# Performance work log

Hardware: AMD Instinct MI355X
Metric: run time of the kernel (lower is better)

## Reference

```python
import jax, jax.numpy as jnp
import numpy as np

N = 50000
E = 800000
F0, F1, F2 = 256, 128, 64
EPS = 1e-5


def setup_inputs() -> dict:
    key = jax.random.key(0)
    ks = jax.random.split(key, 20)
    x = jax.random.normal(ks[0], (N, F0), dtype=jnp.float32)
    src = jax.random.randint(ks[1], (E,), 0, N)
    dst = jax.random.randint(ks[2], (E,), 0, N)
    edge_index = jnp.stack([src, dst]).astype(jnp.int64)

    def lin(k, fi, fo):
        s = 1.0 / np.sqrt(fi)
        k1, k2 = jax.random.split(k)
        W = jax.random.uniform(k1, (fi, fo), minval=-s, maxval=s, dtype=jnp.float32)
        b = jax.random.uniform(k2, (fo,), minval=-s, maxval=s, dtype=jnp.float32)
        return W, b

    We1, be1 = lin(ks[3], F0, F1)
    We2, be2 = lin(ks[4], F1, F2)
    Wd1, bd1 = lin(ks[5], F2, F1)
    Wd2, bd2 = lin(ks[6], F1, F0)
    return {
        'x': x, 'edge_index': edge_index,
        'We1': We1, 'be1': be1, 'g1': jnp.ones((F1,)), 'bb1': jnp.zeros((F1,)),
        'We2': We2, 'be2': be2, 'g2': jnp.ones((F2,)), 'bb2': jnp.zeros((F2,)),
        'Wd1': Wd1, 'bd1': bd1, 'g3': jnp.ones((F1,)), 'bb3': jnp.zeros((F1,)),
        'Wd2': Wd2, 'bd2': bd2, 'g4': jnp.ones((F0,)), 'bb4': jnp.zeros((F0,)),
    }


def _gcn(x, W, b, src, dst, dinv_src_dst, dinv_self):
    # PyG GCNConv: linear first, then sym-normalized propagation with self-loops
    h = x @ W + b                               # [N, Fout]
    msg = h[src] * dinv_src_dst[:, None]        # [E, Fout]
    out = jax.ops.segment_sum(msg, dst, num_segments=N)
    return out + h * dinv_self[:, None]         # self-loop term


def _bn(x, g, b):
    # BatchNorm1d training-mode: biased batch stats over node dim
    m = jnp.mean(x, axis=0)
    v = jnp.mean(jnp.square(x - m), axis=0)
    return g * (x - m) * jax.lax.rsqrt(v + EPS) + b


def reference(x, edge_index, We1, be1, g1, bb1, We2, be2, g2, bb2,
              Wd1, bd1, g3, bb3, Wd2, bd2, g4, bb4):
    src, dst = edge_index[0], edge_index[1]
    deg = jnp.zeros((N,), x.dtype).at[dst].add(1.0) + 1.0  # in-degree + self-loop
    dinv = jax.lax.rsqrt(deg)
    dsd = dinv[src] * dinv[dst]
    dself = dinv * dinv

    relu = jax.nn.relu
    # Encoder block 0 (outer i==0): relu(GCN), relu(BN)
    h = relu(_gcn(x, We1, be1, src, dst, dsd, dself))
    h = relu(_bn(h, g1, bb1))
    enc1 = h
    # Encoder block 1 (outer i==1 == len(inner)-1): relu(GCN), BN (no relu)
    h = relu(_gcn(h, We2, be2, src, dst, dsd, dself))
    h = _bn(h, g2, bb2)
    enc2 = h
    # Decoder block 0: relu(GCN), relu(BN)
    h = relu(_gcn(h, Wd1, bd1, src, dst, dsd, dself))
    h = relu(_bn(h, g3, bb3))
    # Decoder block 1 (i==1): relu(GCN), BN (no relu)
    h = relu(_gcn(h, Wd2, bd2, src, dst, dsd, dself))
    h = _bn(h, g4, bb4)
    # AE returns (reconstruction, encoded_embeddings)
    return h, enc1, enc2
```

## Files before the change

### kernel.cpp

```cpp
#include <hip/hip_runtime.h>

#define N_NODES 50000
#define F0 256
#define F1 128
#define F2 64
#define BN_EPS 1e-5f

typedef float f32x4 __attribute__((ext_vector_type(4)));
typedef __bf16 bf16x8 __attribute__((ext_vector_type(8)));
typedef unsigned short ushort8v __attribute__((ext_vector_type(8)));

__device__ __forceinline__ float bflo(unsigned v) { return __uint_as_float(v << 16); }
__device__ __forceinline__ float bfhi(unsigned v) { return __uint_as_float(v & 0xFFFF0000u); }
__device__ __forceinline__ unsigned short f2bf(float f) {
  unsigned u = __float_as_uint(f);
  u += 0x7FFFu + ((u >> 16) & 1u);
  return (unsigned short)(u >> 16);
}
__device__ __forceinline__ void split2(float a, unsigned short& hi, unsigned short& lo) {
  hi = f2bf(a);
  float hf = __uint_as_float((unsigned)hi << 16);
  lo = f2bf(a - hf);
}
__device__ __forceinline__ int rdl(int v, int l) { return __builtin_amdgcn_readlane(v, l); }
__device__ __forceinline__ float rdlf(float v, int l) {
  return __uint_as_float((unsigned)__builtin_amdgcn_readlane(__float_as_int(v), l));
}

__global__ void count_dst(const int* __restrict__ dst, int* __restrict__ counts, int E) {
  int e = blockIdx.x * blockDim.x + threadIdx.x;
  if (e < E) atomicAdd(&counts[dst[e]], 1);
}

__global__ __launch_bounds__(256) void scan_blocks(const int* __restrict__ counts,
                                                   int* __restrict__ offs,
                                                   int* __restrict__ bsum,
                                                   float* __restrict__ dinv) {
  __shared__ int s_w[4];
  const int tid = threadIdx.x, lane = tid & 63, wid = tid >> 6;
  const int base = blockIdx.x * 1024 + tid * 4;
  int v0 = 0, v1 = 0, v2 = 0, v3 = 0;
  if (base + 3 < N_NODES) {
    int4 v = *(const int4*)(counts + base);
    v0 = v.x; v1 = v.y; v2 = v.z; v3 = v.w;
  } else if (base < N_NODES) {
    v0 = counts[base];
    if (base + 1 < N_NODES) v1 = counts[base + 1];
    if (base + 2 < N_NODES) v2 = counts[base + 2];
  }
  if (base < N_NODES) {
    dinv[base] = rsqrtf((float)v0 + 1.0f);
    if (base + 1 < N_NODES) dinv[base + 1] = rsqrtf((float)v1 + 1.0f);
    if (base + 2 < N_NODES) dinv[base + 2] = rsqrtf((float)v2 + 1.0f);
    if (base + 3 < N_NODES) dinv[base + 3] = rsqrtf((float)v3 + 1.0f);
  }
  int t = v0 + v1 + v2 + v3;
  int incl = t;
#pragma unroll
  for (int d = 1; d < 64; d <<= 1) {
    int x = __shfl_up(incl, d);
    if (lane >= d) incl += x;
  }
  if (lane == 63) s_w[wid] = incl;
  __syncthreads();
  int woff = 0;
#pragma unroll
  for (int j = 0; j < 4; j++)
    if (j < wid) woff += s_w[j];
  int p = woff + incl - t;
  if (base < N_NODES) offs[base] = p;
  p += v0;
  if (base + 1 < N_NODES) offs[base + 1] = p;
  p += v1;
  if (base + 2 < N_NODES) offs[base + 2] = p;
  p += v2;
  if (base + 3 < N_NODES) offs[base + 3] = p;
  if (tid == 255) bsum[blockIdx.x] = woff + incl;
}

__global__ void scan_tops(int* __restrict__ bsum, int* __restrict__ offs, int nblk) {
  int lane = threadIdx.x;
  int v = (lane < nblk) ? bsum[lane] : 0;
  int incl = v;
#pragma unroll
  for (int d = 1; d < 64; d <<= 1) {
    int x = __shfl_up(incl, d);
    if (lane >= d) incl += x;
  }
  if (lane < nblk) bsum[lane] = incl - v;
  if (lane == 63) offs[N_NODES] = incl;
}

__global__ __launch_bounds__(256) void scan_add(int* __restrict__ offs,
                                                const int* __restrict__ bsum,
                                                const float* __restrict__ dinv,
                                                float* __restrict__ rowsum) {
  const int add = bsum[blockIdx.x];
  const int base = blockIdx.x * 1024 + threadIdx.x * 4;
  if (base + 3 < N_NODES) {
    int4 v = *(const int4*)(offs + base);
    v.x += add; v.y += add; v.z += add; v.w += add;
    *(int4*)(offs + base) = v;
    float4 d = *(const float4*)(dinv + base);
    float4 r;
    r.x = d.x * d.x; r.y = d.y * d.y; r.z = d.z * d.z; r.w = d.w * d.w;
    *(float4*)(rowsum + base) = r;
  } else if (base < N_NODES) {
    for (int k = 0; k < 4 && base + k < N_NODES; k++) {
      offs[base + k] += add;
      float d = dinv[base + k];
      rowsum[base + k] = d * d;
    }
  }
}

__global__ void fill_csr(const int* __restrict__ src, const int* __restrict__ dst,
                         const int* __restrict__ offs, int* __restrict__ cursor,
                         const float* __restrict__ dinv,
                         int* __restrict__ csr_src, float* __restrict__ csr_w,
                         float* __restrict__ rowsum, int E) {
  int e = blockIdx.x * blockDim.x + threadIdx.x;
  if (e < E) {
    int s = src[e], d = dst[e];
    int p = offs[d] + atomicAdd(&cursor[d], 1);
    float w = dinv[s] * dinv[d];
    csr_src[p] = s;
    csr_w[p] = w;
    atomicAdd(&rowsum[d], w);
  }
}

__device__ __forceinline__ void wt_one(const float* W, unsigned short* Wh, unsigned short* Wl,
                                       int K, int N, int idx) {
  int k = idx / N, n = idx - k * N;
  unsigned short h, l;
  split2(W[idx], h, l);
  Wh[(size_t)n * K + k] = h;
  Wl[(size_t)n * K + k] = l;
}

__global__ void convert_weights(const float* __restrict__ We1, const float* __restrict__ We2,
                                const float* __restrict__ Wd1, const float* __restrict__ Wd2,
                                unsigned short* W1h, unsigned short* W1l,
                                unsigned short* W2h, unsigned short* W2l,
                                unsigned short* W3h, unsigned short* W3l,
                                unsigned short* W4h, unsigned short* W4l) {
  int idx = blockIdx.x * blockDim.x + threadIdx.x;
  if (idx < 32768) {
    wt_one(We1, W1h, W1l, 256, 128, idx);
  } else if (idx < 40960) {
    wt_one(We2, W2h, W2l, 128, 64, idx - 32768);
  } else if (idx < 49152) {
    wt_one(Wd1, W3h, W3l, 64, 128, idx - 40960);
  } else if (idx < 81920) {
    wt_one(Wd2, W4h, W4l, 128, 256, idx - 49152);
  }
}

template <int BN, bool STATS, bool AF32>
__global__ __launch_bounds__(256) void mfma_gemm_split(
    const unsigned short* __restrict__ Ahi, const unsigned short* __restrict__ Alo,
    const float* __restrict__ Af,
    const unsigned short* __restrict__ Whi, const unsigned short* __restrict__ Wlo,
    const float* __restrict__ bias, const float* __restrict__ rowsum,
    unsigned short* __restrict__ Cb, float* __restrict__ Cf,
    float* __restrict__ stat, int M, int K, int N) {
  constexpr int BM = 128;
  constexpr int MT = (BN == 128) ? 4 : 2;
  constexpr int NT = 4;
  __shared__ __align__(16) unsigned short AsH[4][BM][8];
  __shared__ __align__(16) unsigned short AsL[4][BM][8];
  __shared__ __align__(16) unsigned short BsH[4][BN][8];
  __shared__ __align__(16) unsigned short BsL[4][BN][8];
  const int tid = threadIdx.x;
  const int lane = tid & 63, wid = tid >> 6;
  const int quad = lane >> 4, ln = lane & 15;
  const int m0 = blockIdx.x * BM;
  const int n0 = blockIdx.y * BN;
  const int wm = (BN == 128) ? (wid & 1) * 64 : wid * 32;
  const int wn = (BN == 128) ? (wid >> 1) * 64 : 0;
  f32x4 acc[MT][NT] = {};

  const int arow = tid >> 2, aseg = tid & 3;
  for (int k0 = 0; k0 < K; k0 += 32) {
#pragma unroll
    for (int i = 0; i < 2; i++) {
      int row = arow + i * 64;
      int gm = m0 + row;
      if (AF32) {
        float4 u0 = make_float4(0.f, 0.f, 0.f, 0.f), u1 = u0;
        if (gm < M) {
          u0 = *(const float4*)(Af + (size_t)gm * K + k0 + aseg * 8);
          u1 = *(const float4*)(Af + (size_t)gm * K + k0 + aseg * 8 + 4);
        }
        ushort4 h0, l0, h1, l1;
        split2(u0.x, h0.x, l0.x); split2(u0.y, h0.y, l0.y);
        split2(u0.z, h0.z, l0.z); split2(u0.w, h0.w, l0.w);
        split2(u1.x, h1.x, l1.x); split2(u1.y, h1.y, l1.y);
        split2(u1.z, h1.z, l1.z); split2(u1.w, h1.w, l1.w);
        *(ushort4*)(&AsH[aseg][row][0]) = h0;
        *(ushort4*)(&AsH[aseg][row][4]) = h1;
        *(ushort4*)(&AsL[aseg][row][0]) = l0;
        *(ushort4*)(&AsL[aseg][row][4]) = l1;
      } else {
        ushort8v vh = {0, 0, 0, 0, 0, 0, 0, 0};
        ushort8v vl = {0, 0, 0, 0, 0, 0, 0, 0};
        if (gm < M) {
          vh = *(const ushort8v*)(Ahi + (size_t)gm * K + k0 + aseg * 8);
          vl = *(const ushort8v*)(Alo + (size_t)gm * K + k0 + aseg * 8);
        }
        *(ushort8v*)(&AsH[aseg][row][0]) = vh;
        *(ushort8v*)(&AsL[aseg][row][0]) = vl;
      }
    }
#pragma unroll
    for (int i = 0; i < BN / 64; i++) {
      int n = arow + i * 64;
      *(ushort8v*)(&BsH[aseg][n][0]) =
          *(const ushort8v*)(Whi + (size_t)(n0 + n) * K + k0 + aseg * 8);
      *(ushort8v*)(&BsL[aseg][n][0]) =
          *(const ushort8v*)(Wlo + (size_t)(n0 + n) * K + k0 + aseg * 8);
    }
    __syncthreads();
    bf16x8 ah[MT], al[MT], bh[NT], bl[NT];
#pragma unroll
    for (int mt = 0; mt < MT; mt++) {
      ah[mt] = *(const bf16x8*)(&AsH[quad][wm + mt * 16 + ln][0]);
      al[mt] = *(const bf16x8*)(&AsL[quad][wm + mt * 16 + ln][0]);
    }
#pragma unroll
    for (int nt = 0; nt < NT; nt++) {
      bh[nt] = *(const bf16x8*)(&BsH[quad][wn + nt * 16 + ln][0]);
      bl[nt] = *(const bf16x8*)(&BsL[quad][wn + nt * 16 + ln][0]);
    }
#pragma unroll
    for (int mt = 0; mt < MT; mt++)
#pragma unroll
      for (int nt = 0; nt < NT; nt++) {
        acc[mt][nt] = __builtin_amdgcn_mfma_f32_16x16x32_bf16(ah[mt], bl[nt], acc[mt][nt], 0, 0, 0);
        acc[mt][nt] = __builtin_amdgcn_mfma_f32_16x16x32_bf16(al[mt], bh[nt], acc[mt][nt], 0, 0, 0);
        acc[mt][nt] = __builtin_amdgcn_mfma_f32_16x16x32_bf16(ah[mt], bh[nt], acc[mt][nt], 0, 0, 0);
      }
    __syncthreads();
  }

  if (!STATS) {
#pragma unroll
    for (int nt = 0; nt < NT; nt++) {
      int gn = n0 + wn + nt * 16 + ln;
      float bv = bias[gn];
#pragma unroll
      for (int mt = 0; mt < MT; mt++) {
#pragma unroll
        for (int r = 0; r < 4; r++) {
          int gm = m0 + wm + mt * 16 + quad * 4 + r;
          if (gm < M) Cb[(size_t)gm * N + gn] = f2bf(acc[mt][nt][r] + bv);
        }
      }
    }
  } else {
    float rs[MT][4];
#pragma unroll
    for (int mt = 0; mt < MT; mt++)
#pragma unroll
      for (int r = 0; r < 4; r++) {
        int gm = m0 + wm + mt * 16 + quad * 4 + r;
        rs[mt][r] = (gm < M) ? rowsum[gm] : 0.f;
      }
#pragma unroll
    for (int nt = 0; nt < NT; nt++) {
      int gn = n0 + wn + nt * 16 + ln;
      float bv = bias[gn];
      float ls = 0.f, lq = 0.f;
#pragma unroll
      for (int mt = 0; mt < MT; mt++) {
#pragma unroll
        for (int r = 0; r < 4; r++) {
          int gm = m0 + wm + mt * 16 + quad * 4 + r;
          if (gm < M) {
            float v = fmaxf(fmaf(bv, rs[mt][r], acc[mt][nt][r]), 0.f);
            Cf[(size_t)gm * N + gn] = v;
            ls += v;
            lq = fmaf(v, v, lq);
          }
        }
      }
      ls += __shfl_xor(ls, 16); ls += __shfl_xor(ls, 32);
      lq += __shfl_xor(lq, 16); lq += __shfl_xor(lq, 32);
      if (quad == 0) {
        atomicAdd(&stat[gn], ls);
        atomicAdd(&stat[256 + gn], lq);
      }
    }
  }
}

template <bool RELU_STATS, bool OUT_SPLIT>
__global__ __launch_bounds__(256) void agg128_rl(
    const unsigned short* __restrict__ hb, const int* __restrict__ offs,
    const int* __restrict__ csr_src, const float* __restrict__ csr_w,
    const float* __restrict__ dinv, float* __restrict__ outf,
    unsigned short* __restrict__ outhi, unsigned short* __restrict__ outlo,
    float* __restrict__ stat) {
  const int tid = threadIdx.x;
  const int lane = tid & 63;
  const int widx = tid >> 6;
  const int nwaves = gridDim.x * 4;
  float ls0 = 0.f, ls1 = 0.f, lq0 = 0.f, lq1 = 0.f;

  for (int node = blockIdx.x * 4 + widx; node < N_NODES; node += nwaves) {
    const int e0 = __builtin_amdgcn_readfirstlane(offs[node]);
    const int e1 = __builtin_amdgcn_readfirstlane(offs[node + 1]);
    float a0 = 0.f, a1 = 0.f;
    for (int e = e0; e < e1; e += 64) {
      const int cnt = min(64, e1 - e);
      int idx = 0;
      float wt = 0.f;
      if (lane < cnt) {
        idx = csr_src[e + lane];
        wt = csr_w[e + lane];
      }
      const int nb = (cnt + 7) & ~7;
      for (int j = 0; j < nb; j += 8) {
#pragma unroll
        for (int u = 0; u < 8; u++) {
          int s = rdl(idx, j + u);
          float w = rdlf(wt, j + u);
          unsigned v = *(const unsigned*)(hb + (size_t)s * 128 + lane * 2);
          a0 = fmaf(bflo(v), w, a0);
          a1 = fmaf(bfhi(v), w, a1);
        }
      }
    }
    float di = dinv[node];
    float ds = di * di;
    unsigned vs = *(const unsigned*)(hb + (size_t)node * 128 + lane * 2);
    a0 = fmaf(bflo(vs), ds, a0);
    a1 = fmaf(bfhi(vs), ds, a1);
    if (RELU_STATS) {
      a0 = fmaxf(a0, 0.f);
      a1 = fmaxf(a1, 0.f);
      ls0 += a0; ls1 += a1;
      lq0 = fmaf(a0, a0, lq0);
      lq1 = fmaf(a1, a1, lq1);
    }
    if (OUT_SPLIT) {
      unsigned short h0, l0, h1, l1;
      split2(a0, h0, l0);
      split2(a1, h1, l1);
      *(unsigned*)(outhi + (size_t)node * 128 + lane * 2) = (unsigned)h0 | ((unsigned)h1 << 16);
      *(unsigned*)(outlo + (size_t)node * 128 + lane * 2) = (unsigned)l0 | ((unsigned)l1 << 16);
    } else {
      *(float2*)(outf + (size_t)node * 128 + lane * 2) = make_float2(a0, a1);
    }
  }

  if (RELU_STATS) {
    __shared__ float red[4][128];
    red[widx][lane * 2 + 0] = ls0;
    red[widx][lane * 2 + 1] = ls1;
    __syncthreads();
    if (tid < 128) {
      atomicAdd(&stat[tid], red[0][tid] + red[1][tid] + red[2][tid] + red[3][tid]);
    }
    __syncthreads();
    red[widx][lane * 2 + 0] = lq0;
    red[widx][lane * 2 + 1] = lq1;
    __syncthreads();
    if (tid < 128) {
      atomicAdd(&stat[256 + tid], red[0][tid] + red[1][tid] + red[2][tid] + red[3][tid]);
    }
  }
}

template <bool RELU_STATS, bool OUT_SPLIT>
__global__ __launch_bounds__(256) void agg64_rl(
    const unsigned short* __restrict__ hb, const int* __restrict__ offs,
    const int* __restrict__ csr_src, const float* __restrict__ csr_w,
    const float* __restrict__ dinv, float* __restrict__ outf,
    unsigned short* __restrict__ outhi, unsigned short* __restrict__ outlo,
    float* __restrict__ stat) {
  const int tid = threadIdx.x;
  const int lane = tid & 63;
  const int widx = tid >> 6;
  const int half = lane >> 5;
  const int hl = lane & 31;
  const int nwaves = gridDim.x * 4;
  float ls0 = 0.f, ls1 = 0.f, lq0 = 0.f, lq1 = 0.f;

  for (int node = blockIdx.x * 4 + widx; node < N_NODES; node += nwaves) {
    const int e0 = __builtin_amdgcn_readfirstlane(offs[node]);
    const int e1 = __builtin_amdgcn_readfirstlane(offs[node + 1]);
    float a0 = 0.f, a1 = 0.f;
    for (int e = e0; e < e1; e += 64) {
      const int cnt = min(64, e1 - e);
      int idx = 0;
      float wt = 0.f;
      if (lane < cnt) {
        idx = csr_src[e + lane];
        wt = csr_w[e + lane];
      }
      const int nb = (cnt + 15) & ~15;
      for (int j = 0; j < nb; j += 16) {
#pragma unroll
        for (int u = 0; u < 8; u++) {
          int sa = rdl(idx, j + 2 * u);
          int sb = rdl(idx, j + 2 * u + 1);
          float wa = rdlf(wt, j + 2 * u);
          float wb = rdlf(wt, j + 2 * u + 1);
          const unsigned short* pa = hb + (size_t)sa * 64;
          const unsigned short* pb = hb + (size_t)sb * 64;
          const unsigned short* p = half ? pb : pa;
          float w = half ? wb : wa;
          unsigned v = *(const unsigned*)(p + hl * 2);
          a0 = fmaf(bflo(v), w, a0);
          a1 = fmaf(bfhi(v), w, a1);
        }
      }
    }
    a0 += __shfl_xor(a0, 32);
    a1 += __shfl_xor(a1, 32);
    float di = dinv[node];
    float ds = di * di;
    unsigned vs = *(const unsigned*)(hb + (size_t)node * 64 + hl * 2);
    a0 = fmaf(bflo(vs), ds, a0);
    a1 = fmaf(bfhi(vs), ds, a1);
    if (RELU_STATS) {
      a0 = fmaxf(a0, 0.f);
      a1 = fmaxf(a1, 0.f);
      if (half == 0) {
        ls0 += a0; ls1 += a1;
        lq0 = fmaf(a0, a0, lq0);
        lq1 = fmaf(a1, a1, lq1);
      }
    }
    if (half == 0) {
      if (OUT_SPLIT) {
        unsigned short h0, l0, h1, l1;
        split2(a0, h0, l0);
        split2(a1, h1, l1);
        *(unsigned*)(outhi + (size_t)node * 64 + hl * 2) = (unsigned)h0 | ((unsigned)h1 << 16);
        *(unsigned*)(outlo + (size_t)node * 64 + hl * 2) = (unsigned)l0 | ((unsigned)l1 << 16);
      } else {
        *(float2*)(outf + (size_t)node * 64 + hl * 2) = make_float2(a0, a1);
      }
    }
  }

  if (RELU_STATS) {
    __shared__ float red[4][64];
    if (half == 0) {
      red[widx][hl * 2 + 0] = ls0;
      red[widx][hl * 2 + 1] = ls1;
    }
    __syncthreads();
    if (tid < 64) {
      atomicAdd(&stat[tid], red[0][tid] + red[1][tid] + red[2][tid] + red[3][tid]);
    }
    __syncthreads();
    if (half == 0) {
      red[widx][hl * 2 + 0] = lq0;
      red[widx][hl * 2 + 1] = lq1;
    }
    __syncthreads();
    if (tid < 64) {
      atomicAdd(&stat[256 + tid], red[0][tid] + red[1][tid] + red[2][tid] + red[3][tid]);
    }
  }
}

template <int F, bool RELU, bool WF32, bool WB16, bool WSPLIT>
__global__ __launch_bounds__(256) void bn_apply_f(const float* __restrict__ a,
                                                  const float* __restrict__ stat,
                                                  const float* __restrict__ g,
                                                  const float* __restrict__ bb,
                                                  float* __restrict__ outf,
                                                  unsigned short* __restrict__ outb,
                                                  unsigned short* __restrict__ outhi,
                                                  unsigned short* __restrict__ outlo) {
  __shared__ float s_scale[F], s_shift[F];
  const int tid = threadIdx.x;
  if (tid < F) {
    const float invN = 1.0f / (float)N_NODES;
    float mean = stat[tid] * invN;
    float var = fmaxf(stat[256 + tid] * invN - mean * mean, 0.f);
    float inv = rsqrtf(var + BN_EPS);
    float sc = g[tid] * inv;
    s_scale[tid] = sc;
    s_shift[tid] = bb[tid] - mean * sc;
  }
  __syncthreads();
  constexpr int C4 = F / 4;
  const int total = N_NODES * C4;
  for (int idx = blockIdx.x * blockDim.x + tid; idx < total; idx += gridDim.x * blockDim.x) {
    int c4 = idx % C4;
    float4 v = ((const float4*)a)[idx];
    float4 s = *(float4*)&s_scale[c4 * 4];
    float4 sh = *(float4*)&s_shift[c4 * 4];
    float4 o;
    o.x = fmaf(v.x, s.x, sh.x);
    o.y = fmaf(v.y, s.y, sh.y);
    o.z = fmaf(v.z, s.z, sh.z);
    o.w = fmaf(v.w, s.w, sh.w);
    if (RELU) {
      o.x = fmaxf(o.x, 0.f);
      o.y = fmaxf(o.y, 0.f);
      o.z = fmaxf(o.z, 0.f);
      o.w = fmaxf(o.w, 0.f);
    }
    if (WF32) ((float4*)outf)[idx] = o;
    if (WB16) {
      ushort4 b;
      b.x = f2bf(o.x); b.y = f2bf(o.y); b.z = f2bf(o.z); b.w = f2bf(o.w);
      ((ushort4*)outb)[idx] = b;
    }
    if (WSPLIT) {
      ushort4 h, l;
      split2(o.x, h.x, l.x);
      split2(o.y, h.y, l.y);
      split2(o.z, h.z, l.z);
      split2(o.w, h.w, l.w);
      ((ushort4*)outhi)[idx] = h;
      ((ushort4*)outlo)[idx] = l;
    }
  }
}

extern "C" void kernel_launch(void* const* d_in, const int* in_sizes, int n_in,
                              void* d_out, int out_size, void* d_ws, size_t ws_size,
                              hipStream_t stream) {
  const float* x = (const float*)d_in[0];
  const int* ei = (const int*)d_in[1];
  const int E = in_sizes[1] / 2;
  const int* src = ei;
  const int* dst = ei + E;
  const float* We1 = (const float*)d_in[2];  const float* be1 = (const float*)d_in[3];
  const float* g1  = (const float*)d_in[4];  const float* bb1 = (const float*)d_in[5];
  const float* We2 = (const float*)d_in[6];  const float* be2 = (const float*)d_in[7];
  const float* g2  = (const float*)d_in[8];  const float* bb2 = (const float*)d_in[9];
  const float* Wd1 = (const float*)d_in[10]; const float* bd1 = (const float*)d_in[11];
  const float* g3  = (const float*)d_in[12]; const float* bb3 = (const float*)d_in[13];
  const float* Wd2 = (const float*)d_in[14]; const float* bd2 = (const float*)d_in[15];
  const float* g4  = (const float*)d_in[16]; const float* bb4 = (const float*)d_in[17];

  float* out = (float*)d_out;
  char* ws = (char*)d_ws;
  unsigned short* A0b  = (unsigned short*)(ws + 0);
  unsigned short* A1b  = (unsigned short*)(ws + 12800000);
  unsigned short* C2b  = (unsigned short*)(ws + 32000000);
  unsigned short* G3hi = (unsigned short*)(ws + 0);
  unsigned short* G3lo = (unsigned short*)(ws + 6400000);
  unsigned short* D3b  = (unsigned short*)(ws + 12800000);
  unsigned short* G4hi = (unsigned short*)(ws + 0);
  unsigned short* G4lo = (unsigned short*)(ws + 25600000);
  unsigned short* Wb   = (unsigned short*)(ws + 48000000);
  unsigned short* W1h = Wb;            unsigned short* W1l = W1h + 32768;
  unsigned short* W2h = W1l + 32768;   unsigned short* W2l = W2h + 8192;
  unsigned short* W3h = W2l + 8192;    unsigned short* W3l = W3h + 8192;
  unsigned short* W4h = W3l + 8192;    unsigned short* W4l = W4h + 32768;
  float* B0f  = (float*)(ws + 51200000);
  int*   csrS   = (int*)(ws + 102400000);
  float* csrW   = (float*)(ws + 105600000);
  float* stat4  = (float*)(ws + 108800000);
  int*   bsum   = (int*)(ws + 108808192);
  int*   counts = (int*)(ws + 108810000);
  int*   cursor = (int*)(ws + 109010000);
  int*   offs   = (int*)(ws + 109210000);
  float* dinv   = (float*)(ws + 109410064);
  if (ws_size < 109604160) return;
  float* rowsum = (float*)counts;

  float* enc1 = out + (size_t)N_NODES * F0;
  float* enc2 = enc1 + (size_t)N_NODES * F1;

  const int EB = (E + 255) / 256;
  const int AGG_GRID = 2048;
  const int MB = (N_NODES + 127) / 128;
  const int SCAN_B = (N_NODES + 1023) / 1024;

  convert_weights<<<320, 256, 0, stream>>>(We1, We2, Wd1, Wd2, W1h, W1l, W2h, W2l,
                                           W3h, W3l, W4h, W4l);
  hipMemsetAsync(counts, 0, 400000, stream);
  hipMemsetAsync(stat4, 0, 4 * 512 * sizeof(float), stream);
  count_dst<<<EB, 256, 0, stream>>>(dst, counts, E);
  scan_blocks<<<SCAN_B, 256, 0, stream>>>(counts, offs, bsum, dinv);
  scan_tops<<<1, 64, 0, stream>>>(bsum, offs, SCAN_B);
  scan_add<<<SCAN_B, 256, 0, stream>>>(offs, bsum, dinv, rowsum);
  fill_csr<<<EB, 256, 0, stream>>>(src, dst, offs, cursor, dinv, csrS, csrW, rowsum, E);

  mfma_gemm_split<128, false, true><<<dim3(MB, 1), 256, 0, stream>>>(
      nullptr, nullptr, x, W1h, W1l, be1, nullptr, A0b, nullptr, nullptr, N_NODES, F0, F1);
  agg128_rl<true, false><<<AGG_GRID, 256, 0, stream>>>(
      A0b, offs, csrS, csrW, dinv, B0f, nullptr, nullptr, stat4);
  bn_apply_f<F1, true, true, false, false><<<2048, 256, 0, stream>>>(
      B0f, stat4, g1, bb1, enc1, nullptr, nullptr, nullptr);

  mfma_gemm_split<64, false, true><<<dim3(MB, 1), 256, 0, stream>>>(
      nullptr, nullptr, enc1, W2h, W2l, be2, nullptr, A1b, nullptr, nullptr, N_NODES, F1, F2);
  agg64_rl<true, false><<<AGG_GRID, 256, 0, stream>>>(
      A1b, offs, csrS, csrW, dinv, B0f, nullptr, nullptr, stat4 + 512);
  bn_apply_f<F2, false, true, true, false><<<2048, 256, 0, stream>>>(
      B0f, stat4 + 512, g2, bb2, enc2, C2b, nullptr, nullptr);

  agg64_rl<false, true><<<AGG_GRID, 256, 0, stream>>>(
      C2b, offs, csrS, csrW, dinv, nullptr, G3hi, G3lo, nullptr);
  mfma_gemm_split<128, true, false><<<dim3(MB, 1), 256, 0, stream>>>(
      G3hi, G3lo, nullptr, W3h, W3l, bd1, rowsum, nullptr, B0f, stat4 + 1024, N_NODES, F2, F1);
  bn_apply_f<F1, true, false, true, false><<<2048, 256, 0, stream>>>(
      B0f, stat4 + 1024, g3, bb3, nullptr, D3b, nullptr, nullptr);

  agg128_rl<false, true><<<AGG_GRID, 256, 0, stream>>>(
      D3b, offs, csrS, csrW, dinv, nullptr, G4hi, G4lo, nullptr);
  mfma_gemm_split<128, true, false><<<dim3(MB, 2), 256, 0, stream>>>(
      G4hi, G4lo, nullptr, W4h, W4l, bd2, rowsum, nullptr, B0f, stat4 + 1536, N_NODES, F1, F0);
  bn_apply_f<F0, false, true, false, false><<<2048, 256, 0, stream>>>(
      B0f, stat4 + 1536, g4, bb4, out, nullptr, nullptr, nullptr);
}
```

Baseline: 639.4 us.

## Pack CSR entries as 64-bit pairs and reuse count-phase atomic slots

The count pass now records each edge's atomic slot, so fill_csr no longer needs a second atomic cursor pass or the cursor memset. The CSR source index and weight are packed into one 64-bit entry written with nontemporal stores, so each aggregation kernel does one load per edge instead of two. The atomic rowsum accumulation is replaced by a separate per-node kernel that sums weights from the CSR. This adds a serial per-thread loop in compute_rowsum and an extra launch, and eslot aliases the B0f buffer.

```diff
diff --git a/kernel.cpp b/kernel.cpp
--- a/kernel.cpp
+++ b/kernel.cpp
@@ -27,9 +27,10 @@
   return __uint_as_float((unsigned)__builtin_amdgcn_readlane(__float_as_int(v), l));
 }
 
-__global__ void count_dst(const int* __restrict__ dst, int* __restrict__ counts, int E) {
+__global__ void count_dst(const int* __restrict__ dst, int* __restrict__ counts,
+                          int* __restrict__ eslot, int E) {
   int e = blockIdx.x * blockDim.x + threadIdx.x;
-  if (e < E) atomicAdd(&counts[dst[e]], 1);
+  if (e < E) eslot[e] = atomicAdd(&counts[dst[e]], 1);
 }
 
 __global__ __launch_bounds__(256) void scan_blocks(const int* __restrict__ counts,
@@ -92,41 +93,43 @@
 }
 
 __global__ __launch_bounds__(256) void scan_add(int* __restrict__ offs,
-                                                const int* __restrict__ bsum,
-                                                const float* __restrict__ dinv,
-                                                float* __restrict__ rowsum) {
+                                                const int* __restrict__ bsum) {
   const int add = bsum[blockIdx.x];
   const int base = blockIdx.x * 1024 + threadIdx.x * 4;
   if (base + 3 < N_NODES) {
     int4 v = *(const int4*)(offs + base);
     v.x += add; v.y += add; v.z += add; v.w += add;
     *(int4*)(offs + base) = v;
-    float4 d = *(const float4*)(dinv + base);
-    float4 r;
-    r.x = d.x * d.x; r.y = d.y * d.y; r.z = d.z * d.z; r.w = d.w * d.w;
-    *(float4*)(rowsum + base) = r;
   } else if (base < N_NODES) {
-    for (int k = 0; k < 4 && base + k < N_NODES; k++) {
-      offs[base + k] += add;
-      float d = dinv[base + k];
-      rowsum[base + k] = d * d;
-    }
+    offs[base] += add;
+    if (base + 1 < N_NODES) offs[base + 1] += add;
+    if (base + 2 < N_NODES) offs[base + 2] += add;
   }
 }
 
 __global__ void fill_csr(const int* __restrict__ src, const int* __restrict__ dst,
-                         const int* __restrict__ offs, int* __restrict__ cursor,
+                         const int* __restrict__ offs, const int* __restrict__ eslot,
                          const float* __restrict__ dinv,
-                         int* __restrict__ csr_src, float* __restrict__ csr_w,
-                         float* __restrict__ rowsum, int E) {
+                         unsigned long long* __restrict__ csrP, int E) {
   int e = blockIdx.x * blockDim.x + threadIdx.x;
   if (e < E) {
     int s = src[e], d = dst[e];
-    int p = offs[d] + atomicAdd(&cursor[d], 1);
-    float w = dinv[s] * dinv[d];
-    csr_src[p] = s;
-    csr_w[p] = w;
-    atomicAdd(&rowsum[d], w);
+    int p = offs[d] + eslot[e];
+    unsigned long long ent =
+        (unsigned)s | ((unsigned long long)__float_as_uint(dinv[s] * dinv[d]) << 32);
+    __builtin_nontemporal_store(ent, &csrP[p]);
+  }
+}
+
+__global__ void compute_rowsum(const int* __restrict__ offs,
+                               const unsigned long long* __restrict__ csrP,
+                               const float* __restrict__ dinv, float* __restrict__ rowsum) {
+  int i = blockIdx.x * blockDim.x + threadIdx.x;
+  if (i < N_NODES) {
+    float s = dinv[i] * dinv[i];
+    int e1 = offs[i + 1];
+    for (int e = offs[i]; e < e1; e++) s += __uint_as_float((unsigned)(csrP[e] >> 32));
+    rowsum[i] = s;
   }
 }
 
@@ -298,10 +301,9 @@
 template <bool RELU_STATS, bool OUT_SPLIT>
 __global__ __launch_bounds__(256) void agg128_rl(
     const unsigned short* __restrict__ hb, const int* __restrict__ offs,
-    const int* __restrict__ csr_src, const float* __restrict__ csr_w,
-    const float* __restrict__ dinv, float* __restrict__ outf,
-    unsigned short* __restrict__ outhi, unsigned short* __restrict__ outlo,
-    float* __restrict__ stat) {
+    const unsigned long long* __restrict__ csrP, const float* __restrict__ dinv,
+    float* __restrict__ outf, unsigned short* __restrict__ outhi,
+    unsigned short* __restrict__ outlo, float* __restrict__ stat) {
   const int tid = threadIdx.x;
   const int lane = tid & 63;
   const int widx = tid >> 6;
@@ -317,8 +319,9 @@
       int idx = 0;
       float wt = 0.f;
       if (lane < cnt) {
-        idx = csr_src[e + lane];
-        wt = csr_w[e + lane];
+        unsigned long long c = csrP[e + lane];
+        idx = (int)(unsigned)c;
+        wt = __uint_as_float((unsigned)(c >> 32));
       }
       const int nb = (cnt + 7) & ~7;
       for (int j = 0; j < nb; j += 8) {
@@ -376,10 +379,9 @@
 template <bool RELU_STATS, bool OUT_SPLIT>
 __global__ __launch_bounds__(256) void agg64_rl(
     const unsigned short* __restrict__ hb, const int* __restrict__ offs,
-    const int* __restrict__ csr_src, const float* __restrict__ csr_w,
-    const float* __restrict__ dinv, float* __restrict__ outf,
-    unsigned short* __restrict__ outhi, unsigned short* __restrict__ outlo,
-    float* __restrict__ stat) {
+    const unsigned long long* __restrict__ csrP, const float* __restrict__ dinv,
+    float* __restrict__ outf, unsigned short* __restrict__ outhi,
+    unsigned short* __restrict__ outlo, float* __restrict__ stat) {
   const int tid = threadIdx.x;
   const int lane = tid & 63;
   const int widx = tid >> 6;
@@ -397,8 +399,9 @@
       int idx = 0;
       float wt = 0.f;
       if (lane < cnt) {
-        idx = csr_src[e + lane];
-        wt = csr_w[e + lane];
+        unsigned long long c = csrP[e + lane];
+        idx = (int)(unsigned)c;
+        wt = __uint_as_float((unsigned)(c >> 32));
       }
       const int nb = (cnt + 15) & ~15;
       for (int j = 0; j < nb; j += 16) {
@@ -559,12 +562,11 @@
   unsigned short* W3h = W2l + 8192;    unsigned short* W3l = W3h + 8192;
   unsigned short* W4h = W3l + 8192;    unsigned short* W4l = W4h + 32768;
   float* B0f  = (float*)(ws + 51200000);
-  int*   csrS   = (int*)(ws + 102400000);
-  float* csrW   = (float*)(ws + 105600000);
+  int*   eslot  = (int*)(ws + 51200000);
+  unsigned long long* csrP = (unsigned long long*)(ws + 102400000);
   float* stat4  = (float*)(ws + 108800000);
   int*   bsum   = (int*)(ws + 108808192);
   int*   counts = (int*)(ws + 108810000);
-  int*   cursor = (int*)(ws + 109010000);
   int*   offs   = (int*)(ws + 109210000);
   float* dinv   = (float*)(ws + 109410064);
   if (ws_size < 109604160) return;
@@ -580,37 +582,38 @@
 
   convert_weights<<<320, 256, 0, stream>>>(We1, We2, Wd1, Wd2, W1h, W1l, W2h, W2l,
                                            W3h, W3l, W4h, W4l);
-  hipMemsetAsync(counts, 0, 400000, stream);
+  hipMemsetAsync(counts, 0, N_NODES * sizeof(int), stream);
   hipMemsetAsync(stat4, 0, 4 * 512 * sizeof(float), stream);
-  count_dst<<<EB, 256, 0, stream>>>(dst, counts, E);
+  count_dst<<<EB, 256, 0, stream>>>(dst, counts, eslot, E);
   scan_blocks<<<SCAN_B, 256, 0, stream>>>(counts, offs, bsum, dinv);
   scan_tops<<<1, 64, 0, stream>>>(bsum, offs, SCAN_B);
-  scan_add<<<SCAN_B, 256, 0, stream>>>(offs, bsum, dinv, rowsum);
-  fill_csr<<<EB, 256, 0, stream>>>(src, dst, offs, cursor, dinv, csrS, csrW, rowsum, E);
+  scan_add<<<SCAN_B, 256, 0, stream>>>(offs, bsum);
+  fill_csr<<<EB, 256, 0, stream>>>(src, dst, offs, eslot, dinv, csrP, E);
+  compute_rowsum<<<(N_NODES + 255) / 256, 256, 0, stream>>>(offs, csrP, dinv, rowsum);
 
   mfma_gemm_split<128, false, true><<<dim3(MB, 1), 256, 0, stream>>>(
       nullptr, nullptr, x, W1h, W1l, be1, nullptr, A0b, nullptr, nullptr, N_NODES, F0, F1);
   agg128_rl<true, false><<<AGG_GRID, 256, 0, stream>>>(
-      A0b, offs, csrS, csrW, dinv, B0f, nullptr, nullptr, stat4);
+      A0b, offs, csrP, dinv, B0f, nullptr, nullptr, stat4);
   bn_apply_f<F1, true, true, false, false><<<2048, 256, 0, stream>>>(
       B0f, stat4, g1, bb1, enc1, nullptr, nullptr, nullptr);
 
   mfma_gemm_split<64, false, true><<<dim3(MB, 1), 256, 0, stream>>>(
       nullptr, nullptr, enc1, W2h, W2l, be2, nullptr, A1b, nullptr, nullptr, N_NODES, F1, F2);
   agg64_rl<true, false><<<AGG_GRID, 256, 0, stream>>>(
-      A1b, offs, csrS, csrW, dinv, B0f, nullptr, nullptr, stat4 + 512);
+      A1b, offs, csrP, dinv, B0f, nullptr, nullptr, stat4 + 512);
   bn_apply_f<F2, false, true, true, false><<<2048, 256, 0, stream>>>(
       B0f, stat4 + 512, g2, bb2, enc2, C2b, nullptr, nullptr);
 
   agg64_rl<false, true><<<AGG_GRID, 256, 0, stream>>>(
-      C2b, offs, csrS, csrW, dinv, nullptr, G3hi, G3lo, nullptr);
+      C2b, offs, csrP, dinv, nullptr, G3hi, G3lo, nullptr);
   mfma_gemm_split<128, true, false><<<dim3(MB, 1), 256, 0, stream>>>(
       G3hi, G3lo, nullptr, W3h, W3l, bd1, rowsum, nullptr, B0f, stat4 + 1024, N_NODES, F2, F1);
   bn_apply_f<F1, true, false, true, false><<<2048, 256, 0, stream>>>(
       B0f, stat4 + 1024, g3, bb3, nullptr, D3b, nullptr, nullptr);
 
   agg128_rl<false, true><<<AGG_GRID, 256, 0, stream>>>(
-      D3b, offs, csrS, csrW, dinv, nullptr, G4hi, G4lo, nullptr);
+      D3b, offs, csrP, dinv, nullptr, G4hi, G4lo, nullptr);
   mfma_gemm_split<128, true, false><<<dim3(MB, 2), 256, 0, stream>>>(
       G4hi, G4lo, nullptr, W4h, W4l, bd2, rowsum, nullptr, B0f, stat4 + 1536, N_NODES, F1, F0);
   bn_apply_f<F0, false, true, false, false><<<2048, 256, 0, stream>>>(
```

New measurement: 595.5 us. 6.9% less time.
